# Kernel tuning notes

Hardware: AMD Instinct MI355X
Metric: run time of the kernel (lower is better)

## Reference

```python
import jax, jax.numpy as jnp
import numpy as np

NUM_HEADS = 12
GAT_HEADS = 4
EPS = 1e-5

def _ln(x, g, b):
    m = x.mean(-1, keepdims=True)
    v = ((x - m) ** 2).mean(-1, keepdims=True)
    return (x - m) / jnp.sqrt(v + EPS) * g + b

def _grid_edges(H, W, B):
    # 8-ish connectivity exactly as the Python loops build it: horizontal,
    # vertical, down-right diag, down-left diag (c>0), both directions,
    # replicated per image with node offset. Pure numpy on static shapes.
    idx = np.arange(H * W).reshape(H, W)
    p = [np.stack([idx[:, :-1].ravel(), idx[:, 1:].ravel()], 1),
         np.stack([idx[:-1, :].ravel(), idx[1:, :].ravel()], 1),
         np.stack([idx[:-1, :-1].ravel(), idx[1:, 1:].ravel()], 1),
         np.stack([idx[:-1, 1:-1].ravel(), idx[1:, :-2].ravel()], 1)]
    e = np.concatenate(p, 0)
    e = np.concatenate([e, e[:, ::-1]], 0)  # bidirectional
    e = (e[None] + (np.arange(B) * H * W)[:, None, None]).reshape(-1, 2)
    return jnp.asarray(e[:, 0]), jnp.asarray(e[:, 1])

def _forward(x, ln1_g, ln1_b, proj_w, proj_b, wqkv, bqkv, wo, bo, ln2_g, ln2_b,
             gp_w, gp_b, gat_w, att_src, att_dst, gat_b, ln3_g, ln3_b,
             mlp_w1, mlp_b1, mlp_w2, mlp_b2, fn_g, fn_b):
    B, C, H, W = x.shape
    S = H * W
    E = proj_w.shape[1]
    tok = x.reshape(B, C, S).transpose(0, 2, 1)            # [B,S,C]
    v_in = _ln(tok, ln1_g, ln1_b) @ proj_w + proj_b        # [B,S,E]
    # --- multi-head self-attention (batch_first, eval: no dropout) ---
    qkv = v_in @ wqkv + bqkv
    q, k, v = jnp.split(qkv, 3, axis=-1)
    dh = E // NUM_HEADS
    def heads(t):
        return t.reshape(B, S, NUM_HEADS, dh).transpose(0, 2, 1, 3)
    q, k, v = heads(q), heads(k), heads(v)
    att = jax.nn.softmax(jnp.einsum('bhqd,bhkd->bhqk', q, k) / jnp.sqrt(jnp.float32(dh)), axis=-1)
    o = jnp.einsum('bhqk,bhkd->bhqd', att, v).transpose(0, 2, 1, 3).reshape(B, S, E)
    x_attn = v_in + (o @ wo + bo)                          # residual
    # --- GAT over the pixel-grid graph ---
    N = B * S
    flat = x_attn.reshape(N, E)
    g = _ln(flat, ln2_g, ln2_b) @ gp_w + gp_b
    dg = E // GAT_HEADS
    hN = (g @ gat_w).reshape(N, GAT_HEADS, dg)             # [N,GH,dg]
    src, dst = _grid_edges(H, W, B)
    loops = jnp.arange(N)                                  # PyG add_self_loops=True
    src = jnp.concatenate([src, loops])
    dst = jnp.concatenate([dst, loops])
    a_s = (hN * att_src).sum(-1)                           # [N,GH]
    a_d = (hN * att_dst).sum(-1)
    e = jax.nn.leaky_relu(a_s[src] + a_d[dst], 0.2)        # [Eedges,GH]
    mseg = jax.ops.segment_max(e, dst, num_segments=N)
    ex = jnp.exp(e - mseg[dst])
    den = jax.ops.segment_sum(ex, dst, num_segments=N)
    alpha = ex / den[dst]                                  # softmax over incoming edges
    agg = jax.ops.segment_sum(hN[src] * alpha[..., None], dst, num_segments=N)
    x_gat = jax.nn.elu(agg.reshape(N, E) + gat_b)
    x_after = flat + x_gat                                 # residual
    # --- MLP block ---
    n3 = _ln(x_after, ln3_g, ln3_b)
    mlp = jax.nn.gelu(n3 @ mlp_w1 + mlp_b1, approximate=False) @ mlp_w2 + mlp_b2
    y = _ln(n3 + mlp, fn_g, fn_b)
    return y.reshape(B, H, W, E).transpose(0, 3, 1, 2)     # [B,E,H,W]

def setup_inputs() -> dict:
    key = jax.random.key(0)
    ks = jax.random.split(key, 16)
    B, C, H, W, E = 4, 2048, 32, 32, 768
    f32 = jnp.float32
    def n(k, shape, s=0.02):
        return jax.random.normal(k, shape, f32) * s
    return {
        'x': jax.random.normal(ks[0], (B, C, H, W), f32),
        'ln1_g': jnp.ones(C, f32), 'ln1_b': jnp.zeros(C, f32),
        'proj_w': n(ks[1], (C, E)), 'proj_b': jnp.zeros(E, f32),
        'wqkv': n(ks[2], (E, 3 * E)), 'bqkv': jnp.zeros(3 * E, f32),
        'wo': n(ks[3], (E, E)), 'bo': jnp.zeros(E, f32),
        'ln2_g': jnp.ones(E, f32), 'ln2_b': jnp.zeros(E, f32),
        'gp_w': n(ks[4], (E, E)), 'gp_b': jnp.zeros(E, f32),
        'gat_w': n(ks[5], (E, E)),
        'att_src': n(ks[6], (GAT_HEADS, E // GAT_HEADS), 0.1),
        'att_dst': n(ks[7], (GAT_HEADS, E // GAT_HEADS), 0.1),
        'gat_b': jnp.zeros(E, f32),
        'ln3_g': jnp.ones(E, f32), 'ln3_b': jnp.zeros(E, f32),
        'mlp_w1': n(ks[8], (E, E)), 'mlp_b1': jnp.zeros(E, f32),
        'mlp_w2': n(ks[9], (E, E)), 'mlp_b2': jnp.zeros(E, f32),
        'fn_g': jnp.ones(E, f32), 'fn_b': jnp.zeros(E, f32),
    }

def reference(x, ln1_g, ln1_b, proj_w, proj_b, wqkv, bqkv, wo, bo, ln2_g, ln2_b,
              gp_w, gp_b, gat_w, att_src, att_dst, gat_b, ln3_g, ln3_b,
              mlp_w1, mlp_b1, mlp_w2, mlp_b2, fn_g, fn_b):
    return _forward(x, ln1_g, ln1_b, proj_w, proj_b, wqkv, bqkv, wo, bo, ln2_g, ln2_b,
                    gp_w, gp_b, gat_w, att_src, att_dst, gat_b, ln3_g, ln3_b,
                    mlp_w1, mlp_b1, mlp_w2, mlp_b2, fn_g, fn_b)
```

## Files before the change

### kernel.cpp

```cpp
#include <hip/hip_runtime.h>

constexpr int Bc = 4;
constexpr int Cc = 2048;
constexpr int Sc = 1024;
constexpr int Ntok = 4096;
constexpr int Ec = 768;
constexpr int E3 = 2304;
constexpr int NHEAD = 12;
constexpr int GHEAD = 4;
constexpr int DGAT = 192;

typedef __attribute__((ext_vector_type(8))) short short8_t;
typedef __attribute__((ext_vector_type(4))) short short4_t;
typedef __attribute__((ext_vector_type(8))) unsigned short u16x8;
typedef __attribute__((ext_vector_type(4))) float f32x4;

__device__ inline unsigned short f2bf(float f) {
  unsigned int u = __builtin_bit_cast(unsigned int, f);
  u += 0x7FFFu + ((u >> 16) & 1u);
  return (unsigned short)(u >> 16);
}
__device__ inline float bf2f(unsigned short h) {
  unsigned int u = ((unsigned int)h) << 16;
  return __builtin_bit_cast(float, u);
}

struct WtArgs {
  const float* src[7];
  unsigned short* dst[7];
  int K[7], N[7];
  int off[8];
};
__global__ __launch_bounds__(256) void k_wt(WtArgs a) {
  __shared__ float t[32][33];
  int bid = blockIdx.x;
  int w = 0;
  while (w < 6 && bid >= a.off[w + 1]) ++w;
  int local = bid - a.off[w];
  int K = a.K[w], N = a.N[w];
  int ntn = N >> 5;
  int tk = local / ntn, tn = local - tk * ntn;
  int k0 = tk * 32, n0 = tn * 32;
  int tx = threadIdx.x & 31, ty = threadIdx.x >> 5;
  const float* src = a.src[w];
#pragma unroll
  for (int i = 0; i < 4; i++)
    t[ty + i * 8][tx] = src[(size_t)(k0 + ty + i * 8) * N + n0 + tx];
  __syncthreads();
  unsigned short* dst = a.dst[w];
#pragma unroll
  for (int i = 0; i < 4; i++)
    dst[(size_t)(n0 + ty + i * 8) * K + k0 + tx] = f2bf(t[tx][ty + i * 8]);
}

__global__ __launch_bounds__(256) void k_ln1_stats(const float* __restrict__ x,
    float* __restrict__ psum, float* __restrict__ pss) {
  int cc = blockIdx.x, st = blockIdx.y, b = blockIdx.z;
  int sl = threadIdx.x & 15, cl = threadIdx.x >> 4;
  int s = st * 16 + sl;
  const float* xb = x + (size_t)b * Cc * Sc + s;
  float sum = 0.f, ss = 0.f;
#pragma unroll
  for (int t = 0; t < 16; t++) {
    int c = cc * 256 + cl + t * 16;
    float v = xb[(size_t)c * Sc];
    sum += v; ss += v * v;
  }
  __shared__ float rs0[16][17], rs1[16][17];
  rs0[cl][sl] = sum; rs1[cl][sl] = ss;
  __syncthreads();
  if (cl == 0) {
    float a = 0.f, q = 0.f;
#pragma unroll
    for (int i = 0; i < 16; i++) { a += rs0[i][sl]; q += rs1[i][sl]; }
    size_t bs = (size_t)(b * Sc + st * 16 + sl);
    psum[bs * 8 + cc] = a;
    pss[bs * 8 + cc] = q;
  }
}

__global__ __launch_bounds__(256) void k_ln1_norm(const float* __restrict__ x,
    const float* __restrict__ g, const float* __restrict__ bt,
    const float* __restrict__ psum, const float* __restrict__ pss,
    unsigned short* __restrict__ out) {
  int cc = blockIdx.x, st = blockIdx.y, b = blockIdx.z;
  int sl = threadIdx.x & 15, cl = threadIdx.x >> 4;
  int s = st * 16 + sl;
  __shared__ float red[16][17];
  __shared__ float mean_s[16], rstd_s[16];
  int t8 = cl;
  size_t bsrow = (size_t)(b * Sc + st * 16 + sl);
  float v = (t8 < 8) ? psum[bsrow * 8 + t8] : pss[bsrow * 8 + (t8 - 8)];
  red[t8][sl] = v;
  __syncthreads();
  if (threadIdx.x < 16) {
    float s0 = 0.f, s1 = 0.f;
#pragma unroll
    for (int i = 0; i < 8; i++) { s0 += red[i][threadIdx.x]; s1 += red[i + 8][threadIdx.x]; }
    float mean = s0 / Cc;
    mean_s[threadIdx.x] = mean;
    rstd_s[threadIdx.x] = rsqrtf(s1 / Cc - mean * mean + 1e-5f);
  }
  __syncthreads();
  float mean = mean_s[sl], rstd = rstd_s[sl];
  const float* xb = x + (size_t)b * Cc * Sc + s;
  __shared__ unsigned short Tc[16][136];
  int cb = cc * 128;
#pragma unroll
  for (int t = 0; t < 8; t++) {
    int c = cb + cl + t * 16;
    float xv = xb[(size_t)c * Sc];
    Tc[sl][cl + t * 16] = f2bf((xv - mean) * rstd * g[c] + bt[c]);
  }
  __syncthreads();
  int rl = threadIdx.x >> 4, el = threadIdx.x & 15;
  unsigned short* ob = out + ((size_t)(b * Sc) + st * 16 + rl) * Cc + cb;
  *(u16x8*)&ob[el * 8] = *(const u16x8*)&Tc[rl][el * 8];
}

template<int EPI, int OUTM>
__global__ __launch_bounds__(512) void gemm_bf16(
    const unsigned short* __restrict__ A, const unsigned short* __restrict__ Bt,
    const float* __restrict__ bias, const float* __restrict__ res,
    float* __restrict__ Cf, unsigned short* __restrict__ Cb,
    int M, int N, int K) {
  __shared__ unsigned short As[128][72];
  __shared__ unsigned short Bs[128][72];
  int tid = threadIdx.x;
  int w = tid >> 6, lane = tid & 63, g = lane >> 4, l16 = lane & 15;
  int wm = w >> 2, wn = w & 3;
  int m0 = blockIdx.y * 128, n0 = blockIdx.x * 128;
  int r0 = tid >> 3, ch0 = (tid & 7) * 8;
  int r1 = r0 + 64;
  const unsigned short* Arow0 = A + (size_t)(m0 + r0) * K + ch0;
  const unsigned short* Arow1 = A + (size_t)(m0 + r1) * K + ch0;
  const unsigned short* Brow0 = Bt + (size_t)(n0 + r0) * K + ch0;
  const unsigned short* Brow1 = Bt + (size_t)(n0 + r1) * K + ch0;
  u16x8 ra0 = *(const u16x8*)Arow0;
  u16x8 ra1 = *(const u16x8*)Arow1;
  u16x8 rb0 = *(const u16x8*)Brow0;
  u16x8 rb1 = *(const u16x8*)Brow1;
  f32x4 acc[4][2] = {};
  for (int k0 = 0; k0 < K; k0 += 64) {
    __syncthreads();
    *(u16x8*)&As[r0][ch0] = ra0;
    *(u16x8*)&As[r1][ch0] = ra1;
    *(u16x8*)&Bs[r0][ch0] = rb0;
    *(u16x8*)&Bs[r1][ch0] = rb1;
    __syncthreads();
    if (k0 + 64 < K) {
      ra0 = *(const u16x8*)(Arow0 + k0 + 64);
      ra1 = *(const u16x8*)(Arow1 + k0 + 64);
      rb0 = *(const u16x8*)(Brow0 + k0 + 64);
      rb1 = *(const u16x8*)(Brow1 + k0 + 64);
    }
#pragma unroll
    for (int ks = 0; ks < 2; ks++) {
      short8_t af[4], bf[2];
#pragma unroll
      for (int i = 0; i < 4; i++)
        af[i] = *(const short8_t*)&As[wm * 64 + i * 16 + l16][ks * 32 + g * 8];
#pragma unroll
      for (int j = 0; j < 2; j++)
        bf[j] = *(const short8_t*)&Bs[wn * 32 + j * 16 + l16][ks * 32 + g * 8];
#pragma unroll
      for (int mi = 0; mi < 4; mi++)
#pragma unroll
        for (int ni = 0; ni < 2; ni++)
          acc[mi][ni] = __builtin_amdgcn_mfma_f32_16x16x32_bf16(af[mi], bf[ni], acc[mi][ni], 0, 0, 0);
    }
  }
#pragma unroll
  for (int mi = 0; mi < 4; mi++) {
#pragma unroll
    for (int ni = 0; ni < 2; ni++) {
      int n = n0 + wn * 32 + ni * 16 + l16;
      float bv = 0.f;
      if (EPI != 0) bv = bias[n];
#pragma unroll
      for (int r = 0; r < 4; r++) {
        int m = m0 + wm * 64 + mi * 16 + g * 4 + r;
        float c = acc[mi][ni][r] + bv;
        if (EPI == 2) c += res[(size_t)m * N + n];
        if (EPI == 3) c = 0.5f * c * (1.f + erff(c * 0.70710678118f));
        if (OUTM & 1) Cf[(size_t)m * N + n] = c;
        if (OUTM & 2) Cb[(size_t)m * N + n] = f2bf(c);
      }
    }
  }
}

__global__ __launch_bounds__(256) void k_attn_mfma(const unsigned short* __restrict__ qkv,
    unsigned short* __restrict__ o) {
  __shared__ unsigned short Ks[64][72];
  __shared__ unsigned short Vs[4608];
  __shared__ unsigned short Plb[4][16][72];
  int qt = blockIdx.x, h = blockIdx.y, b = blockIdx.z;
  int tid = threadIdx.x;
  int w = tid >> 6, lane = tid & 63;
  int g = lane >> 4, l16 = lane & 15;
  const unsigned short* base  = qkv + (size_t)b * Sc * E3;
  const unsigned short* kbase = base + Ec + h * 64;
  const unsigned short* vbase = base + 2 * Ec + h * 64;
  int q0 = qt * 64 + w * 16;

  short8_t qf[2];
#pragma unroll
  for (int ks = 0; ks < 2; ks++) {
    short8_t f = *(const short8_t*)&base[(size_t)(q0 + l16) * E3 + h * 64 + ks * 32 + g * 8];
#pragma unroll
    for (int e = 0; e < 8; e++)
      f[e] = (short)f2bf(bf2f((unsigned short)f[e]) * 0.125f);
    qf[ks] = f;
  }

  int r0s = tid >> 3, ch0s = (tid & 7) * 8;
  int r1s = ((tid + 256) >> 3), ch1s = ch0s;
  int voff0 = (r0s >> 2) * 288 + (ch0s >> 4) * 72 + (r0s & 3) * 16 + ((ch0s >> 3) & 1) * 8;
  int voff1 = (r1s >> 2) * 288 + (ch1s >> 4) * 72 + (r1s & 3) * 16 + ((ch1s >> 3) & 1) * 8;
  const unsigned short* krow0 = kbase + (size_t)r0s * E3 + ch0s;
  const unsigned short* krow1 = kbase + (size_t)r1s * E3 + ch1s;
  const unsigned short* vrow0 = vbase + (size_t)r0s * E3 + ch0s;
  const unsigned short* vrow1 = vbase + (size_t)r1s * E3 + ch1s;
  constexpr size_t KTS = (size_t)64 * E3;

  u16x8 rk0 = *(const u16x8*)krow0;
  u16x8 rk1 = *(const u16x8*)krow1;
  u16x8 rv0 = *(const u16x8*)vrow0;
  u16x8 rv1 = *(const u16x8*)vrow1;

  f32x4 o_acc[4] = {};
  float m_r[4] = {-1e30f, -1e30f, -1e30f, -1e30f};
  float l_r[4] = {};

  for (int kt = 0; kt < 16; kt++) {
    __syncthreads();
    *(u16x8*)&Ks[r0s][ch0s] = rk0;
    *(u16x8*)&Ks[r1s][ch1s] = rk1;
    *(u16x8*)&Vs[voff0] = rv0;
    *(u16x8*)&Vs[voff1] = rv1;
    __syncthreads();
    if (kt < 15) {
      size_t off = (size_t)(kt + 1) * KTS;
      rk0 = *(const u16x8*)(krow0 + off);
      rk1 = *(const u16x8*)(krow1 + off);
      rv0 = *(const u16x8*)(vrow0 + off);
      rv1 = *(const u16x8*)(vrow1 + off);
    }

    f32x4 s_acc[4] = {};
#pragma unroll
    for (int nt = 0; nt < 4; nt++) {
#pragma unroll
      for (int ks = 0; ks < 2; ks++) {
        short8_t kf = *(const short8_t*)&Ks[nt * 16 + l16][ks * 32 + g * 8];
        s_acc[nt] = __builtin_amdgcn_mfma_f32_16x16x32_bf16(qf[ks], kf, s_acc[nt], 0, 0, 0);
      }
    }

#pragma unroll
    for (int r = 0; r < 4; r++) {
      float mx = fmaxf(fmaxf(s_acc[0][r], s_acc[1][r]), fmaxf(s_acc[2][r], s_acc[3][r]));
#pragma unroll
      for (int off = 8; off; off >>= 1) mx = fmaxf(mx, __shfl_xor(mx, off));
      float mn = fmaxf(m_r[r], mx);
      float sc = __expf(m_r[r] - mn);
      m_r[r] = mn;
      l_r[r] *= sc;
#pragma unroll
      for (int dt = 0; dt < 4; dt++) o_acc[dt][r] *= sc;
      float ts = 0.f;
#pragma unroll
      for (int nt = 0; nt < 4; nt++) {
        float p = __expf(s_acc[nt][r] - mn);
        s_acc[nt][r] = p;
        ts += p;
      }
#pragma unroll
      for (int off = 8; off; off >>= 1) ts += __shfl_xor(ts, off);
      l_r[r] += ts;
    }

#pragma unroll
    for (int nt = 0; nt < 4; nt++)
#pragma unroll
      for (int r = 0; r < 4; r++)
        Plb[w][g * 4 + r][nt * 16 + l16] = f2bf(s_acc[nt][r]);

#pragma unroll
    for (int ks = 0; ks < 2; ks++) {
      short8_t pf = *(const short8_t*)&Plb[w][l16][ks * 32 + g * 8];
      short4_t lo0, lo1, lo2, lo3, hi0, hi1, hi2, hi3;
      unsigned a0 = (unsigned)(uintptr_t)&Vs[(ks * 8 + g * 2) * 288 + 0 * 72 + l16] * 1u;
      unsigned a1 = a0 + 144, a2 = a0 + 288, a3 = a0 + 432;
      asm volatile("ds_read_b64_tr_b16 %0, %1" : "=v"(lo0) : "v"(a0));
      asm volatile("ds_read_b64_tr_b16 %0, %1 offset:576" : "=v"(hi0) : "v"(a0));
      asm volatile("ds_read_b64_tr_b16 %0, %1" : "=v"(lo1) : "v"(a1));
      asm volatile("ds_read_b64_tr_b16 %0, %1 offset:576" : "=v"(hi1) : "v"(a1));
      asm volatile("ds_read_b64_tr_b16 %0, %1" : "=v"(lo2) : "v"(a2));
      asm volatile("ds_read_b64_tr_b16 %0, %1 offset:576" : "=v"(hi2) : "v"(a2));
      asm volatile("ds_read_b64_tr_b16 %0, %1" : "=v"(lo3) : "v"(a3));
      asm volatile("ds_read_b64_tr_b16 %0, %1 offset:576" : "=v"(hi3) : "v"(a3));
      asm volatile("s_waitcnt lgkmcnt(0)");
      __builtin_amdgcn_sched_barrier(0);
      short4_t lo[4] = {lo0, lo1, lo2, lo3};
      short4_t hi[4] = {hi0, hi1, hi2, hi3};
#pragma unroll
      for (int dt = 0; dt < 4; dt++) {
        short8_t vf;
#pragma unroll
        for (int e = 0; e < 4; e++) { vf[e] = lo[dt][e]; vf[4 + e] = hi[dt][e]; }
        o_acc[dt] = __builtin_amdgcn_mfma_f32_16x16x32_bf16(pf, vf, o_acc[dt], 0, 0, 0);
      }
    }
  }

  unsigned short* obase = o + (size_t)(b * Sc + q0) * Ec + h * 64;
#pragma unroll
  for (int r = 0; r < 4; r++) {
    float inv = 1.f / l_r[r];
    int qrow = g * 4 + r;
#pragma unroll
    for (int dt = 0; dt < 4; dt++)
      obase[(size_t)qrow * Ec + dt * 16 + l16] = f2bf(o_acc[dt][r] * inv);
  }
}

template<int MODE>
__global__ __launch_bounds__(256) void k_lnrow(const float* __restrict__ in,
    const float* __restrict__ g, const float* __restrict__ bt,
    float* __restrict__ outf, unsigned short* __restrict__ outb) {
  int row = blockIdx.x;
  int tid = threadIdx.x;
  __shared__ float buf[Ec];
  __shared__ float rsum[4], rss[4];
  float sum = 0.f, ss = 0.f;
  for (int i = tid; i < Ec; i += 256) {
    float v = in[(size_t)row * Ec + i];
    buf[i] = v; sum += v; ss += v * v;
  }
#pragma unroll
  for (int off = 32; off > 0; off >>= 1) {
    sum += __shfl_xor(sum, off); ss += __shfl_xor(ss, off);
  }
  if ((tid & 63) == 0) { rsum[tid >> 6] = sum; rss[tid >> 6] = ss; }
  __syncthreads();
  sum = rsum[0] + rsum[1] + rsum[2] + rsum[3];
  ss = rss[0] + rss[1] + rss[2] + rss[3];
  float mean = sum / Ec;
  float rstd = rsqrtf(ss / Ec - mean * mean + 1e-5f);
  for (int i = tid; i < Ec; i += 256) {
    float v = (buf[i] - mean) * rstd * g[i] + bt[i];
    if (MODE == 2) outf[(size_t)row * Ec + i] = v;
    outb[(size_t)row * Ec + i] = f2bf(v);
  }
}

__global__ __launch_bounds__(256) void k_lnout(const float* __restrict__ in,
    const float* __restrict__ res, const float* __restrict__ g,
    const float* __restrict__ bt, float* __restrict__ out) {
  int r0 = blockIdx.x * 16;
  int b = r0 >> 10, s0 = r0 & 1023;
  __shared__ float Tr[16][772];
  __shared__ float mean_s[16], rstd_s[16];
  int rl = threadIdx.x >> 4, el = threadIdx.x & 15;
  const float* ip = in + (size_t)(r0 + rl) * Ec;
  const float* rp = res + (size_t)(r0 + rl) * Ec;
  float sum = 0.f, ss = 0.f;
  for (int i = el; i < Ec; i += 16) {
    float v = ip[i] + rp[i];
    Tr[rl][i] = v; sum += v; ss += v * v;
  }
#pragma unroll
  for (int off = 8; off; off >>= 1) {
    sum += __shfl_xor(sum, off); ss += __shfl_xor(ss, off);
  }
  if (el == 0) {
    float mean = sum / Ec;
    mean_s[rl] = mean;
    rstd_s[rl] = rsqrtf(ss / Ec - mean * mean + 1e-5f);
  }
  __syncthreads();
  int sl = threadIdx.x & 15, il = threadIdx.x >> 4;
  float mean = mean_s[sl], rstd = rstd_s[sl];
  for (int i = il; i < Ec; i += 16)
    out[((size_t)b * Ec + i) * Sc + s0 + sl] = (Tr[sl][i] - mean) * rstd * g[i] + bt[i];
}

__global__ __launch_bounds__(256) void k_asd(const float* __restrict__ hN,
    const float* __restrict__ att_src, const float* __restrict__ att_dst,
    float* __restrict__ a_s, float* __restrict__ a_d) {
  int n = blockIdx.x * 4 + (threadIdx.x >> 6);
  int lane = threadIdx.x & 63;
  const float* hrow = hN + (size_t)n * Ec;
#pragma unroll
  for (int h = 0; h < GHEAD; h++) {
    float ps = 0.f, pd = 0.f;
    for (int d = lane; d < DGAT; d += 64) {
      float v = hrow[h * DGAT + d];
      ps += v * att_src[h * DGAT + d];
      pd += v * att_dst[h * DGAT + d];
    }
#pragma unroll
    for (int off = 32; off > 0; off >>= 1) {
      ps += __shfl_xor(ps, off); pd += __shfl_xor(pd, off);
    }
    if (lane == 0) { a_s[n * GHEAD + h] = ps; a_d[n * GHEAD + h] = pd; }
  }
}

__global__ __launch_bounds__(256) void k_gat(const float* __restrict__ hN,
    const float* __restrict__ a_s, const float* __restrict__ a_d,
    const float* __restrict__ x_attn, const float* __restrict__ gat_b,
    float* __restrict__ x_after) {
  int n = blockIdx.x;
  int b = n >> 10, s = n & 1023, r = s >> 5, c = s & 31;
  __shared__ int nbr[9];
  __shared__ float alpha[GHEAD][9];
  int tid = threadIdx.x;
  if (tid < 9) {
    int dr = tid / 3 - 1, dc = tid % 3 - 1;
    int rr = r + dr, cc = c + dc;
    int ok = (rr >= 0 && rr < 32 && cc >= 0 && cc < 32);
    if (dr == -1 && dc == 1 && cc == 31) ok = 0;
    if (dr == 1 && dc == -1 && c == 31) ok = 0;
    nbr[tid] = ok ? ((b << 10) + (rr << 5) + cc) : -1;
  }
  __syncthreads();
  if (tid < GHEAD) {
    int h = tid;
    float ad = a_d[n * GHEAD + h];
    float ev[9]; float m = -1e30f;
#pragma unroll
    for (int j = 0; j < 9; j++) {
      if (nbr[j] >= 0) {
        float e = a_s[nbr[j] * GHEAD + h] + ad;
        e = e > 0.f ? e : 0.2f * e;
        ev[j] = e; m = fmaxf(m, e);
      } else ev[j] = -1e30f;
    }
    float den = 0.f;
#pragma unroll
    for (int j = 0; j < 9; j++) {
      float x = (nbr[j] >= 0) ? expf(ev[j] - m) : 0.f;
      ev[j] = x; den += x;
    }
    float inv = 1.f / den;
#pragma unroll
    for (int j = 0; j < 9; j++) alpha[h][j] = ev[j] * inv;
  }
  __syncthreads();
  for (int e = tid; e < Ec; e += 256) {
    int h = e / DGAT;
    float acc = 0.f;
#pragma unroll
    for (int j = 0; j < 9; j++) {
      int nj = nbr[j];
      if (nj >= 0) acc += alpha[h][j] * hN[(size_t)nj * Ec + e];
    }
    float v = acc + gat_b[e];
    v = v > 0.f ? v : expf(v) - 1.f;
    x_after[(size_t)n * Ec + e] = x_attn[(size_t)n * Ec + e] + v;
  }
}

extern "C" void kernel_launch(void* const* d_in, const int* in_sizes, int n_in,
                              void* d_out, int out_size, void* d_ws, size_t ws_size,
                              hipStream_t stream) {
  (void)in_sizes; (void)n_in; (void)out_size; (void)ws_size;
  const float* x      = (const float*)d_in[0];
  const float* ln1_g  = (const float*)d_in[1];
  const float* ln1_b  = (const float*)d_in[2];
  const float* proj_w = (const float*)d_in[3];
  const float* proj_b = (const float*)d_in[4];
  const float* wqkv   = (const float*)d_in[5];
  const float* bqkv   = (const float*)d_in[6];
  const float* wo     = (const float*)d_in[7];
  const float* bo     = (const float*)d_in[8];
  const float* ln2_g  = (const float*)d_in[9];
  const float* ln2_b  = (const float*)d_in[10];
  const float* gp_w   = (const float*)d_in[11];
  const float* gp_b   = (const float*)d_in[12];
  const float* gat_w  = (const float*)d_in[13];
  const float* att_src= (const float*)d_in[14];
  const float* att_dst= (const float*)d_in[15];
  const float* gat_b  = (const float*)d_in[16];
  const float* ln3_g  = (const float*)d_in[17];
  const float* ln3_b  = (const float*)d_in[18];
  const float* mlp_w1 = (const float*)d_in[19];
  const float* mlp_b1 = (const float*)d_in[20];
  const float* mlp_w2 = (const float*)d_in[21];
  const float* mlp_b2 = (const float*)d_in[22];
  const float* fn_g   = (const float*)d_in[23];
  const float* fn_b   = (const float*)d_in[24];
  float* out = (float*)d_out;

  char* p = (char*)d_ws;
  auto alloc = [&](size_t bytes) { char* q = p; p += (bytes + 255) & ~(size_t)255; return q; };
  char* regA      = alloc((size_t)Ntok * E3 * 2);
  unsigned short* n1_bf  = (unsigned short*)regA;
  unsigned short* qkv_bf = (unsigned short*)regA;
  unsigned short* proj_wt = (unsigned short*)alloc((size_t)Ec * Cc * 2);
  unsigned short* wqkv_t  = (unsigned short*)alloc((size_t)E3 * Ec * 2);
  unsigned short* wo_t    = (unsigned short*)alloc((size_t)Ec * Ec * 2);
  unsigned short* gp_t    = (unsigned short*)alloc((size_t)Ec * Ec * 2);
  unsigned short* gat_t   = (unsigned short*)alloc((size_t)Ec * Ec * 2);
  unsigned short* m1_t    = (unsigned short*)alloc((size_t)Ec * Ec * 2);
  unsigned short* m2_t    = (unsigned short*)alloc((size_t)Ec * Ec * 2);
  float* v_in   = (float*)alloc((size_t)Ntok * Ec * 4);
  unsigned short* v_in_bf = (unsigned short*)alloc((size_t)Ntok * Ec * 2);
  unsigned short* regE    = (unsigned short*)alloc((size_t)Ntok * Ec * 2);
  float* regF   = (float*)alloc((size_t)Ntok * Ec * 4);
  unsigned short* regG    = (unsigned short*)alloc((size_t)Ntok * Ec * 2);
  unsigned short* g_bf    = (unsigned short*)alloc((size_t)Ntok * Ec * 2);
  float* hN     = (float*)alloc((size_t)Ntok * Ec * 4);
  float* regJ   = (float*)alloc((size_t)Ntok * Ec * 4);
  float* a_s    = (float*)alloc((size_t)Ntok * GHEAD * 4);
  float* a_d    = (float*)alloc((size_t)Ntok * GHEAD * 4);
  float* psum   = (float*)alloc((size_t)Ntok * 8 * 4);
  float* pss    = (float*)alloc((size_t)Ntok * 8 * 4);

  unsigned short* o_bf   = regE;
  unsigned short* h1_bf  = regE;
  float* x_attn = regF;
  float* n3_f   = regF;
  unsigned short* n2_bf  = regG;
  unsigned short* n3_bf  = regG;
  float* x_after = regJ;
  float* mlp_out = regJ;

  WtArgs wa;
  wa.src[0] = proj_w; wa.dst[0] = proj_wt; wa.K[0] = Cc; wa.N[0] = Ec;
  wa.src[1] = wqkv;   wa.dst[1] = wqkv_t;  wa.K[1] = Ec; wa.N[1] = E3;
  wa.src[2] = wo;     wa.dst[2] = wo_t;    wa.K[2] = Ec; wa.N[2] = Ec;
  wa.src[3] = gp_w;   wa.dst[3] = gp_t;    wa.K[3] = Ec; wa.N[3] = Ec;
  wa.src[4] = gat_w;  wa.dst[4] = gat_t;   wa.K[4] = Ec; wa.N[4] = Ec;
  wa.src[5] = mlp_w1; wa.dst[5] = m1_t;    wa.K[5] = Ec; wa.N[5] = Ec;
  wa.src[6] = mlp_w2; wa.dst[6] = m2_t;    wa.K[6] = Ec; wa.N[6] = Ec;
  int cum = 0;
  for (int i = 0; i < 7; i++) { wa.off[i] = cum; cum += (wa.K[i] >> 5) * (wa.N[i] >> 5); }
  wa.off[7] = cum;
  k_wt<<<cum, 256, 0, stream>>>(wa);

  k_ln1_stats<<<dim3(8, 64, 4), 256, 0, stream>>>(x, psum, pss);
  k_ln1_norm<<<dim3(16, 64, 4), 256, 0, stream>>>(x, ln1_g, ln1_b, psum, pss, n1_bf);
  gemm_bf16<1, 3><<<dim3(Ec / 128, Ntok / 128), 512, 0, stream>>>(
      n1_bf, proj_wt, proj_b, nullptr, v_in, v_in_bf, Ntok, Ec, Cc);
  gemm_bf16<1, 2><<<dim3(E3 / 128, Ntok / 128), 512, 0, stream>>>(
      v_in_bf, wqkv_t, bqkv, nullptr, nullptr, qkv_bf, Ntok, E3, Ec);
  k_attn_mfma<<<dim3(16, NHEAD, Bc), 256, 0, stream>>>(qkv_bf, o_bf);
  gemm_bf16<2, 1><<<dim3(Ec / 128, Ntok / 128), 512, 0, stream>>>(
      o_bf, wo_t, bo, v_in, x_attn, nullptr, Ntok, Ec, Ec);
  k_lnrow<0><<<Ntok, 256, 0, stream>>>(x_attn, ln2_g, ln2_b, nullptr, n2_bf);
  gemm_bf16<1, 2><<<dim3(Ec / 128, Ntok / 128), 512, 0, stream>>>(
      n2_bf, gp_t, gp_b, nullptr, nullptr, g_bf, Ntok, Ec, Ec);
  gemm_bf16<0, 1><<<dim3(Ec / 128, Ntok / 128), 512, 0, stream>>>(
      g_bf, gat_t, nullptr, nullptr, hN, nullptr, Ntok, Ec, Ec);
  k_asd<<<Ntok / 4, 256, 0, stream>>>(hN, att_src, att_dst, a_s, a_d);
  k_gat<<<Ntok, 256, 0, stream>>>(hN, a_s, a_d, x_attn, gat_b, x_after);
  k_lnrow<2><<<Ntok, 256, 0, stream>>>(x_after, ln3_g, ln3_b, n3_f, n3_bf);
  gemm_bf16<3, 2><<<dim3(Ec / 128, Ntok / 128), 512, 0, stream>>>(
      n3_bf, m1_t, mlp_b1, nullptr, nullptr, h1_bf, Ntok, Ec, Ec);
  gemm_bf16<1, 1><<<dim3(Ec / 128, Ntok / 128), 512, 0, stream>>>(
      h1_bf, m2_t, mlp_b2, nullptr, mlp_out, nullptr, Ntok, Ec, Ec);
  k_lnout<<<256, 256, 0, stream>>>(n3_f, mlp_out, fn_g, fn_b, out);
}
```

Before: 265.6 us.

## Fold gp projection into GAT weight and transpose attention score layout

Precomputes the product gp_w·gat_w and the folded bias gp_b·gat_w once per call, so the two back-to-back 4096x768x768 GEMMs become one GEMM plus a small 768x768x768 weight GEMM and a bias reduction. Separately, the attention kernel swaps the MFMA operand order so each lane holds one query row's scores, which reduces the per-row shuffle reductions and lets P be written to LDS as packed pairs. The folding changes rounding, since the combined weight is computed and stored in bf16 and the intermediate bf16 activation g is no longer produced. It also adds a few small kernels to the setup work.

```diff
diff --git a/kernel.cpp b/kernel.cpp
--- a/kernel.cpp
+++ b/kernel.cpp
@@ -28,7 +28,7 @@
 struct WtArgs {
   const float* src[7];
   unsigned short* dst[7];
-  int K[7], N[7];
+  int K[7], N[7], mode[7];
   int off[8];
 };
 __global__ __launch_bounds__(256) void k_wt(WtArgs a) {
@@ -43,14 +43,40 @@
   int k0 = tk * 32, n0 = tn * 32;
   int tx = threadIdx.x & 31, ty = threadIdx.x >> 5;
   const float* src = a.src[w];
+  unsigned short* dst = a.dst[w];
+  if (a.mode[w]) {
+#pragma unroll
+    for (int i = 0; i < 4; i++)
+      dst[(size_t)(k0 + ty + i * 8) * N + n0 + tx] =
+          f2bf(src[(size_t)(k0 + ty + i * 8) * N + n0 + tx]);
+    return;
+  }
 #pragma unroll
   for (int i = 0; i < 4; i++)
     t[ty + i * 8][tx] = src[(size_t)(k0 + ty + i * 8) * N + n0 + tx];
   __syncthreads();
-  unsigned short* dst = a.dst[w];
 #pragma unroll
   for (int i = 0; i < 4; i++)
     dst[(size_t)(n0 + ty + i * 8) * K + k0 + tx] = f2bf(t[tx][ty + i * 8]);
+}
+
+__global__ __launch_bounds__(256) void k_bias2p(const float* __restrict__ gat_w,
+    const float* __restrict__ gp_b, float* __restrict__ part) {
+  int m = blockIdx.x * 256 + threadIdx.x;
+  int jc = blockIdx.y;
+  float acc = 0.f;
+#pragma unroll 8
+  for (int j = jc * 96; j < jc * 96 + 96; j++)
+    acc += gp_b[j] * gat_w[(size_t)j * Ec + m];
+  part[jc * Ec + m] = acc;
+}
+__global__ __launch_bounds__(256) void k_bias2r(const float* __restrict__ part,
+    float* __restrict__ bias2) {
+  int m = blockIdx.x * 256 + threadIdx.x;
+  float acc = 0.f;
+#pragma unroll
+  for (int j = 0; j < 8; j++) acc += part[j * Ec + m];
+  bias2[m] = acc;
 }
 
 __global__ __launch_bounds__(256) void k_ln1_stats(const float* __restrict__ x,
@@ -215,13 +241,13 @@
   }
 
   int r0s = tid >> 3, ch0s = (tid & 7) * 8;
-  int r1s = ((tid + 256) >> 3), ch1s = ch0s;
+  int r1s = r0s + 32;
   int voff0 = (r0s >> 2) * 288 + (ch0s >> 4) * 72 + (r0s & 3) * 16 + ((ch0s >> 3) & 1) * 8;
-  int voff1 = (r1s >> 2) * 288 + (ch1s >> 4) * 72 + (r1s & 3) * 16 + ((ch1s >> 3) & 1) * 8;
+  int voff1 = (r1s >> 2) * 288 + (ch0s >> 4) * 72 + (r1s & 3) * 16 + ((ch0s >> 3) & 1) * 8;
   const unsigned short* krow0 = kbase + (size_t)r0s * E3 + ch0s;
-  const unsigned short* krow1 = kbase + (size_t)r1s * E3 + ch1s;
+  const unsigned short* krow1 = kbase + (size_t)r1s * E3 + ch0s;
   const unsigned short* vrow0 = vbase + (size_t)r0s * E3 + ch0s;
-  const unsigned short* vrow1 = vbase + (size_t)r1s * E3 + ch1s;
+  const unsigned short* vrow1 = vbase + (size_t)r1s * E3 + ch0s;
   constexpr size_t KTS = (size_t)64 * E3;
 
   u16x8 rk0 = *(const u16x8*)krow0;
@@ -230,13 +256,12 @@
   u16x8 rv1 = *(const u16x8*)vrow1;
 
   f32x4 o_acc[4] = {};
-  float m_r[4] = {-1e30f, -1e30f, -1e30f, -1e30f};
-  float l_r[4] = {};
+  float m_r = -1e30f, l_r = 0.f;
 
   for (int kt = 0; kt < 16; kt++) {
     __syncthreads();
     *(u16x8*)&Ks[r0s][ch0s] = rk0;
-    *(u16x8*)&Ks[r1s][ch1s] = rk1;
+    *(u16x8*)&Ks[r1s][ch0s] = rk1;
     *(u16x8*)&Vs[voff0] = rv0;
     *(u16x8*)&Vs[voff1] = rv1;
     __syncthreads();
@@ -254,38 +279,50 @@
 #pragma unroll
       for (int ks = 0; ks < 2; ks++) {
         short8_t kf = *(const short8_t*)&Ks[nt * 16 + l16][ks * 32 + g * 8];
-        s_acc[nt] = __builtin_amdgcn_mfma_f32_16x16x32_bf16(qf[ks], kf, s_acc[nt], 0, 0, 0);
+        s_acc[nt] = __builtin_amdgcn_mfma_f32_16x16x32_bf16(kf, qf[ks], s_acc[nt], 0, 0, 0);
       }
     }
 
-#pragma unroll
-    for (int r = 0; r < 4; r++) {
-      float mx = fmaxf(fmaxf(s_acc[0][r], s_acc[1][r]), fmaxf(s_acc[2][r], s_acc[3][r]));
-#pragma unroll
-      for (int off = 8; off; off >>= 1) mx = fmaxf(mx, __shfl_xor(mx, off));
-      float mn = fmaxf(m_r[r], mx);
-      float sc = __expf(m_r[r] - mn);
-      m_r[r] = mn;
-      l_r[r] *= sc;
-#pragma unroll
-      for (int dt = 0; dt < 4; dt++) o_acc[dt][r] *= sc;
-      float ts = 0.f;
-#pragma unroll
-      for (int nt = 0; nt < 4; nt++) {
-        float p = __expf(s_acc[nt][r] - mn);
-        s_acc[nt][r] = p;
-        ts += p;
+    float mx = s_acc[0][0];
+#pragma unroll
+    for (int nt = 0; nt < 4; nt++)
+#pragma unroll
+      for (int r = 0; r < 4; r++) mx = fmaxf(mx, s_acc[nt][r]);
+    mx = fmaxf(mx, __shfl_xor(mx, 16));
+    mx = fmaxf(mx, __shfl_xor(mx, 32));
+    float mn = fmaxf(m_r, mx);
+    float sc = __expf(m_r - mn);
+    m_r = mn;
+    float ts = 0.f;
+#pragma unroll
+    for (int nt = 0; nt < 4; nt++)
+#pragma unroll
+      for (int r = 0; r < 4; r++) {
+        float pv = __expf(s_acc[nt][r] - mn);
+        s_acc[nt][r] = pv;
+        ts += pv;
       }
-#pragma unroll
-      for (int off = 8; off; off >>= 1) ts += __shfl_xor(ts, off);
-      l_r[r] += ts;
-    }
-
-#pragma unroll
-    for (int nt = 0; nt < 4; nt++)
-#pragma unroll
-      for (int r = 0; r < 4; r++)
-        Plb[w][g * 4 + r][nt * 16 + l16] = f2bf(s_acc[nt][r]);
+    ts += __shfl_xor(ts, 16);
+    ts += __shfl_xor(ts, 32);
+    l_r = l_r * sc + ts;
+
+    float osc[4];
+#pragma unroll
+    for (int r = 0; r < 4; r++) osc[r] = __shfl(sc, g * 4 + r);
+#pragma unroll
+    for (int dt = 0; dt < 4; dt++)
+#pragma unroll
+      for (int r = 0; r < 4; r++) o_acc[dt][r] *= osc[r];
+
+#pragma unroll
+    for (int nt = 0; nt < 4; nt++) {
+#pragma unroll
+      for (int rp = 0; rp < 2; rp++) {
+        unsigned pk = (unsigned)f2bf(s_acc[nt][rp * 2])
+                    | ((unsigned)f2bf(s_acc[nt][rp * 2 + 1]) << 16);
+        *(unsigned*)&Plb[w][l16][nt * 16 + g * 4 + rp * 2] = pk;
+      }
+    }
 
 #pragma unroll
     for (int ks = 0; ks < 2; ks++) {
@@ -315,14 +352,17 @@
     }
   }
 
+  float linv = 1.f / l_r;
+  float inv4[4];
+#pragma unroll
+  for (int r = 0; r < 4; r++) inv4[r] = __shfl(linv, g * 4 + r);
   unsigned short* obase = o + (size_t)(b * Sc + q0) * Ec + h * 64;
 #pragma unroll
   for (int r = 0; r < 4; r++) {
-    float inv = 1.f / l_r[r];
     int qrow = g * 4 + r;
 #pragma unroll
     for (int dt = 0; dt < 4; dt++)
-      obase[(size_t)qrow * Ec + dt * 16 + l16] = f2bf(o_acc[dt][r] * inv);
+      obase[(size_t)qrow * Ec + dt * 16 + l16] = f2bf(o_acc[dt][r] * inv4[r]);
   }
 }
 
@@ -503,16 +543,18 @@
   unsigned short* proj_wt = (unsigned short*)alloc((size_t)Ec * Cc * 2);
   unsigned short* wqkv_t  = (unsigned short*)alloc((size_t)E3 * Ec * 2);
   unsigned short* wo_t    = (unsigned short*)alloc((size_t)Ec * Ec * 2);
-  unsigned short* gp_t    = (unsigned short*)alloc((size_t)Ec * Ec * 2);
+  unsigned short* gp_bf   = (unsigned short*)alloc((size_t)Ec * Ec * 2);
   unsigned short* gat_t   = (unsigned short*)alloc((size_t)Ec * Ec * 2);
   unsigned short* m1_t    = (unsigned short*)alloc((size_t)Ec * Ec * 2);
   unsigned short* m2_t    = (unsigned short*)alloc((size_t)Ec * Ec * 2);
+  unsigned short* gpgat_t = (unsigned short*)alloc((size_t)Ec * Ec * 2);
+  float* bias2p = (float*)alloc((size_t)8 * Ec * 4);
+  float* bias2  = (float*)alloc((size_t)Ec * 4);
   float* v_in   = (float*)alloc((size_t)Ntok * Ec * 4);
   unsigned short* v_in_bf = (unsigned short*)alloc((size_t)Ntok * Ec * 2);
   unsigned short* regE    = (unsigned short*)alloc((size_t)Ntok * Ec * 2);
   float* regF   = (float*)alloc((size_t)Ntok * Ec * 4);
   unsigned short* regG    = (unsigned short*)alloc((size_t)Ntok * Ec * 2);
-  unsigned short* g_bf    = (unsigned short*)alloc((size_t)Ntok * Ec * 2);
   float* hN     = (float*)alloc((size_t)Ntok * Ec * 4);
   float* regJ   = (float*)alloc((size_t)Ntok * Ec * 4);
   float* a_s    = (float*)alloc((size_t)Ntok * GHEAD * 4);
@@ -530,17 +572,22 @@
   float* mlp_out = regJ;
 
   WtArgs wa;
-  wa.src[0] = proj_w; wa.dst[0] = proj_wt; wa.K[0] = Cc; wa.N[0] = Ec;
-  wa.src[1] = wqkv;   wa.dst[1] = wqkv_t;  wa.K[1] = Ec; wa.N[1] = E3;
-  wa.src[2] = wo;     wa.dst[2] = wo_t;    wa.K[2] = Ec; wa.N[2] = Ec;
-  wa.src[3] = gp_w;   wa.dst[3] = gp_t;    wa.K[3] = Ec; wa.N[3] = Ec;
-  wa.src[4] = gat_w;  wa.dst[4] = gat_t;   wa.K[4] = Ec; wa.N[4] = Ec;
-  wa.src[5] = mlp_w1; wa.dst[5] = m1_t;    wa.K[5] = Ec; wa.N[5] = Ec;
-  wa.src[6] = mlp_w2; wa.dst[6] = m2_t;    wa.K[6] = Ec; wa.N[6] = Ec;
+  wa.src[0] = proj_w; wa.dst[0] = proj_wt; wa.K[0] = Cc; wa.N[0] = Ec;  wa.mode[0] = 0;
+  wa.src[1] = wqkv;   wa.dst[1] = wqkv_t;  wa.K[1] = Ec; wa.N[1] = E3;  wa.mode[1] = 0;
+  wa.src[2] = wo;     wa.dst[2] = wo_t;    wa.K[2] = Ec; wa.N[2] = Ec;  wa.mode[2] = 0;
+  wa.src[3] = gat_w;  wa.dst[3] = gat_t;   wa.K[3] = Ec; wa.N[3] = Ec;  wa.mode[3] = 0;
+  wa.src[4] = mlp_w1; wa.dst[4] = m1_t;    wa.K[4] = Ec; wa.N[4] = Ec;  wa.mode[4] = 0;
+  wa.src[5] = mlp_w2; wa.dst[5] = m2_t;    wa.K[5] = Ec; wa.N[5] = Ec;  wa.mode[5] = 0;
+  wa.src[6] = gp_w;   wa.dst[6] = gp_bf;   wa.K[6] = Ec; wa.N[6] = Ec;  wa.mode[6] = 1;
   int cum = 0;
   for (int i = 0; i < 7; i++) { wa.off[i] = cum; cum += (wa.K[i] >> 5) * (wa.N[i] >> 5); }
   wa.off[7] = cum;
   k_wt<<<cum, 256, 0, stream>>>(wa);
+
+  k_bias2p<<<dim3(3, 8), 256, 0, stream>>>(gat_w, gp_b, bias2p);
+  k_bias2r<<<3, 256, 0, stream>>>(bias2p, bias2);
+  gemm_bf16<0, 2><<<dim3(Ec / 128, Ec / 128), 512, 0, stream>>>(
+      gat_t, gp_bf, nullptr, nullptr, nullptr, gpgat_t, Ec, Ec, Ec);
 
   k_ln1_stats<<<dim3(8, 64, 4), 256, 0, stream>>>(x, psum, pss);
   k_ln1_norm<<<dim3(16, 64, 4), 256, 0, stream>>>(x, ln1_g, ln1_b, psum, pss, n1_bf);
@@ -552,10 +599,8 @@
   gemm_bf16<2, 1><<<dim3(Ec / 128, Ntok / 128), 512, 0, stream>>>(
       o_bf, wo_t, bo, v_in, x_attn, nullptr, Ntok, Ec, Ec);
   k_lnrow<0><<<Ntok, 256, 0, stream>>>(x_attn, ln2_g, ln2_b, nullptr, n2_bf);
-  gemm_bf16<1, 2><<<dim3(Ec / 128, Ntok / 128), 512, 0, stream>>>(
-      n2_bf, gp_t, gp_b, nullptr, nullptr, g_bf, Ntok, Ec, Ec);
-  gemm_bf16<0, 1><<<dim3(Ec / 128, Ntok / 128), 512, 0, stream>>>(
-      g_bf, gat_t, nullptr, nullptr, hN, nullptr, Ntok, Ec, Ec);
+  gemm_bf16<1, 1><<<dim3(Ec / 128, Ntok / 128), 512, 0, stream>>>(
+      n2_bf, gpgat_t, bias2, nullptr, hN, nullptr, Ntok, Ec, Ec);
   k_asd<<<Ntok / 4, 256, 0, stream>>>(hN, att_src, att_dst, a_s, a_d);
   k_gat<<<Ntok, 256, 0, stream>>>(hN, a_s, a_d, x_attn, gat_b, x_after);
   k_lnrow<2><<<Ntok, 256, 0, stream>>>(x_after, ln3_g, ln3_b, n3_f, n3_bf);
```

Result: no change. 260.5 us (-1.9%).
